# Performance work log

Hardware: AMD Instinct MI355X
Metric: run time of the kernel (lower is better)

The kernel has to match this reference:

```python
import jax, jax.numpy as jnp
import numpy as np

N_NODES = 512      # num_nodes (seq_len for LSTM, also output side length)
B = 64             # graph batch -> total nodes = B * N_NODES
T = B * N_NODES    # 32768 total nodes
E = 1048576        # edges before self-loops
D_IN = 128
H = 128
L = 2              # lstm layers


def setup_inputs() -> dict:
    key = jax.random.key(0)
    ks = jax.random.split(key, 12)
    x = jax.random.normal(ks[0], (T, D_IN), dtype=jnp.float32)
    edge_index = jax.random.randint(ks[1], (2, E), 0, T, dtype=jnp.int64)
    edge_weight = jax.random.uniform(ks[2], (E,), dtype=jnp.float32)
    batch = jax.random.randint(ks[3], (T,), 0, B, dtype=jnp.int64)
    s = 1.0 / np.sqrt(H)
    W_gcn = jax.random.normal(ks[4], (D_IN, H), dtype=jnp.float32) * s
    b_gcn = jnp.zeros((H,), dtype=jnp.float32)
    w_ih = jax.random.uniform(ks[5], (L, 4 * H, H), minval=-s, maxval=s, dtype=jnp.float32)
    w_hh = jax.random.uniform(ks[6], (L, 4 * H, H), minval=-s, maxval=s, dtype=jnp.float32)
    b_ih = jax.random.uniform(ks[7], (L, 4 * H), minval=-s, maxval=s, dtype=jnp.float32)
    b_hh = jax.random.uniform(ks[8], (L, 4 * H), minval=-s, maxval=s, dtype=jnp.float32)
    fc_w = jax.random.uniform(ks[9], (N_NODES * N_NODES, H), minval=-s, maxval=s, dtype=jnp.float32)
    fc_b = jax.random.uniform(ks[10], (N_NODES * N_NODES,), minval=-s, maxval=s, dtype=jnp.float32)
    return {"x": x, "edge_index": edge_index, "edge_weight": edge_weight, "batch": batch,
            "W_gcn": W_gcn, "b_gcn": b_gcn, "w_ih": w_ih, "w_hh": w_hh,
            "b_ih": b_ih, "b_hh": b_hh, "fc_w": fc_w, "fc_b": fc_b}


def _gcn_conv(x, edge_index, edge_weight, W, b):
    # PyG GCNConv with edge weights: add self-loops (w=1), symmetric norm, then aggregate.
    n = x.shape[0]
    loop = jnp.arange(n, dtype=edge_index.dtype)
    src = jnp.concatenate([edge_index[0], loop])
    dst = jnp.concatenate([edge_index[1], loop])
    w = jnp.concatenate([edge_weight, jnp.ones((n,), dtype=edge_weight.dtype)])
    deg = jax.ops.segment_sum(w, dst, num_segments=n)
    dinv = jnp.where(deg > 0, jax.lax.rsqrt(jnp.maximum(deg, 1e-30)), 0.0)
    norm = dinv[src] * w * dinv[dst]                  # [E+n]
    xw = x @ W                                        # [n, H]
    msg = norm[:, None] * xw[src]                     # gather + scale
    out = jax.ops.segment_sum(msg, dst, num_segments=n)  # scatter-add
    return out + b


def _lstm_layer(xs, wih, whh, bih, bhh):
    # xs: [S, B, H] time-major; torch gate order i,f,g,o.
    h0 = jnp.zeros((xs.shape[1], whh.shape[1]), dtype=xs.dtype)
    c0 = jnp.zeros_like(h0)
    def step(carry, xt):
        h, c = carry
        gates = xt @ wih.T + h @ whh.T + bih + bhh
        i, f, g, o = jnp.split(gates, 4, axis=-1)
        c = jax.nn.sigmoid(f) * c + jax.nn.sigmoid(i) * jnp.tanh(g)
        h = jax.nn.sigmoid(o) * jnp.tanh(c)
        return (h, c), h
    _, hs = jax.lax.scan(step, (h0, c0), xs)
    return hs


def reference(x, edge_index, edge_weight, batch, W_gcn, b_gcn, w_ih, w_hh, b_ih, b_hh, fc_w, fc_b):
    h = _gcn_conv(x, edge_index, edge_weight, W_gcn, b_gcn)   # [T, H]
    # split into chunks of num_nodes and stack -> [B, N_NODES, H]
    h = h.reshape(B, N_NODES, H)
    xs = jnp.transpose(h, (1, 0, 2))                           # [S, B, H]
    for l in range(L):
        xs = _lstm_layer(xs, w_ih[l], w_hh[l], b_ih[l], b_hh[l])
    last = xs[-1]                                              # [B, H]
    out = last @ fc_w.T + fc_b                                 # [B, N_NODES^2]
    return out.reshape(N_NODES, -1)
```

## Files before the change

### kernel.cpp

```cpp
#include <hip/hip_runtime.h>

#define TNODES 32768
#define NEDGE  1048576
#define HD     128
#define NG     512
#define NB     64
#define SEQ    512
#define FCN    262144

__global__ __launch_bounds__(256) void k_deg(const int* __restrict__ ei,
                                             const float* __restrict__ ew,
                                             float* __restrict__ deg,
                                             int* __restrict__ cnt) {
    int e = blockIdx.x * 256 + threadIdx.x;
    int d = ei[NEDGE + e];
    atomicAdd(&deg[d], ew[e]);
    atomicAdd(&cnt[d], 1);
}

__global__ __launch_bounds__(256) void k_dinv(float* __restrict__ deg) {
    int n = blockIdx.x * 256 + threadIdx.x;
    deg[n] = rsqrtf(deg[n] + 1.0f);
}

__global__ __launch_bounds__(1024) void k_scan(const int* __restrict__ cnt,
                                               int* __restrict__ offs) {
    __shared__ int sums[1024];
    int t = threadIdx.x;
    int base = t * 32;
    int local[32];
    int s = 0;
    #pragma unroll
    for (int j = 0; j < 32; ++j) { local[j] = s; s += cnt[base + j]; }
    sums[t] = s;
    __syncthreads();
    for (int off = 1; off < 1024; off <<= 1) {
        int v = sums[t];
        int u = (t >= off) ? sums[t - off] : 0;
        __syncthreads();
        sums[t] = v + u;
        __syncthreads();
    }
    int baseSum = (t == 0) ? 0 : sums[t - 1];
    #pragma unroll
    for (int j = 0; j < 32; ++j) offs[base + j] = baseSum + local[j];
    if (t == 1023) offs[TNODES] = sums[1023];
}

__global__ __launch_bounds__(256) void k_fill(const int* __restrict__ ei,
                                              const float* __restrict__ ew,
                                              const float* __restrict__ dinv,
                                              const int* __restrict__ offs,
                                              int* __restrict__ cursor,
                                              int* __restrict__ csrc,
                                              float* __restrict__ ca) {
    int e = blockIdx.x * 256 + threadIdx.x;
    int s = ei[e];
    int d = ei[NEDGE + e];
    int p = offs[d] + atomicAdd(&cursor[d], 1);
    csrc[p] = s;
    ca[p] = ew[e] * dinv[s];
}

__global__ __launch_bounds__(256) void k_transpose(const float* __restrict__ W,
                                                   float* __restrict__ Wt) {
    int t = blockIdx.x * 256 + threadIdx.x;
    int c = t >> 7, k = t & 127;
    Wt[t] = W[k * HD + c];
}

#define GS 140
__global__ __launch_bounds__(256) void k_gemm_bt(const float* __restrict__ A,
                                                 const float* __restrict__ Bt,
                                                 const float* __restrict__ b1,
                                                 const float* __restrict__ b2,
                                                 float* __restrict__ C, int G) {
    __shared__ __align__(16) float As[64 * GS];
    __shared__ __align__(16) float Bs[64 * GS];
    int r0 = blockIdx.x * 64;
    int g0 = blockIdx.y * 64;
    int tid = threadIdx.x;
    #pragma unroll
    for (int it = 0; it < 8; ++it) {
        int idx = tid + 256 * it;
        int r = idx >> 5, c4 = idx & 31;
        float4 va = ((const float4*)(A + (size_t)(r0 + r) * HD))[c4];
        *((float4*)&As[r * GS + c4 * 4]) = va;
        float4 vb = ((const float4*)(Bt + (size_t)(g0 + r) * HD))[c4];
        *((float4*)&Bs[r * GS + c4 * 4]) = vb;
    }
    __syncthreads();
    int i = tid >> 4;
    int j = tid & 15;
    float acc[4][4];
    #pragma unroll
    for (int a = 0; a < 4; ++a)
        #pragma unroll
        for (int b = 0; b < 4; ++b) acc[a][b] = 0.f;
    #pragma unroll 8
    for (int k4 = 0; k4 < 32; ++k4) {
        float4 av[4], bv[4];
        #pragma unroll
        for (int mi = 0; mi < 4; ++mi)
            av[mi] = *((const float4*)&As[(i + 16 * mi) * GS + k4 * 4]);
        #pragma unroll
        for (int ni = 0; ni < 4; ++ni)
            bv[ni] = *((const float4*)&Bs[(j + 16 * ni) * GS + k4 * 4]);
        #pragma unroll
        for (int mi = 0; mi < 4; ++mi)
            #pragma unroll
            for (int ni = 0; ni < 4; ++ni)
                acc[mi][ni] += (av[mi].x * bv[ni].x + av[mi].y * bv[ni].y) +
                               (av[mi].z * bv[ni].z + av[mi].w * bv[ni].w);
    }
    #pragma unroll
    for (int mi = 0; mi < 4; ++mi)
        #pragma unroll
        for (int ni = 0; ni < 4; ++ni) {
            int g = g0 + j + 16 * ni;
            float bias = (b1 ? b1[g] : 0.f) + (b2 ? b2[g] : 0.f);
            C[(size_t)(r0 + i + 16 * mi) * G + g] = acc[mi][ni] + bias;
        }
}

__global__ __launch_bounds__(128) void k_agg(const int* __restrict__ offs,
                                             const int* __restrict__ csrc,
                                             const float* __restrict__ ca,
                                             const float* __restrict__ xw,
                                             const float* __restrict__ dinv,
                                             const float* __restrict__ bg,
                                             float* __restrict__ hg) {
    int d = blockIdx.x;
    int t = threadIdx.x;
    int beg = offs[d], end = offs[d + 1];
    float acc = 0.f;
    int e = beg;
    for (; e + 3 < end; e += 4) {
        int s0 = csrc[e], s1 = csrc[e + 1], s2 = csrc[e + 2], s3 = csrc[e + 3];
        float a0 = ca[e], a1 = ca[e + 1], a2 = ca[e + 2], a3 = ca[e + 3];
        acc += a0 * xw[(size_t)s0 * HD + t];
        acc += a1 * xw[(size_t)s1 * HD + t];
        acc += a2 * xw[(size_t)s2 * HD + t];
        acc += a3 * xw[(size_t)s3 * HD + t];
    }
    for (; e < end; ++e) acc += ca[e] * xw[(size_t)csrc[e] * HD + t];
    float di = dinv[d];
    hg[(size_t)d * HD + t] = di * acc + di * di * xw[(size_t)d * HD + t] + bg[t];
}

__device__ __forceinline__ float sigm(float x) { return 1.f / (1.f + __expf(-x)); }
__device__ __forceinline__ float tanh_s(float x) {
    float e = __expf(-2.f * fabsf(x));
    float t = (1.f - e) / (1.f + e);
    return copysignf(t, x);
}

#define COMP(v, j) ((j) == 0 ? (v).x : ((j) == 1 ? (v).y : ((j) == 2 ? (v).z : (v).w)))

__global__ __launch_bounds__(512, 2) void k_lstm(const float* __restrict__ P,
                                                 const float* __restrict__ whh,
                                                 float* __restrict__ Hout,
                                                 float* __restrict__ lastOut) {
    __shared__ __align__(16) float lds[20608];
    float* h_sh = lds + 18432;
    int b = blockIdx.x, t = threadIdx.x;
    int c = t >> 7;
    int i = t & 127;

    float4 w[4][8];
    for (int cc = 0; cc < 4; ++cc) {
        const float4* src = (const float4*)(whh + (size_t)t * HD + 32 * cc);
        float4 tmp[8];
        #pragma unroll
        for (int q = 0; q < 8; ++q) tmp[q] = src[q];
        __syncthreads();
        #pragma unroll
        for (int q = 0; q < 8; ++q)
            *((float4*)(lds + t * 36 + 4 * q)) = tmp[q];
        __syncthreads();
        if (cc == c) {
            #pragma unroll
            for (int g = 0; g < 4; ++g)
                #pragma unroll
                for (int q = 0; q < 8; ++q)
                    w[g][q] = *((const float4*)(lds + (i + 128 * g) * 36 + 4 * q));
        }
    }
    __syncthreads();

    if (t < HD) h_sh[t] = 0.f;
    float cst = 0.f;
    const float* Pb = P + (size_t)b * SEQ * NG;
    float pi = 0.f, pf = 0.f, pg = 0.f, po = 0.f;
    if (t < HD) { pi = Pb[t]; pf = Pb[128 + t]; pg = Pb[256 + t]; po = Pb[384 + t]; }
    __syncthreads();

    for (int s = 0; s < SEQ; ++s) {
        float pi2 = 0.f, pf2 = 0.f, pg2 = 0.f, po2 = 0.f;
        if (t < HD && s + 1 < SEQ) {
            const float* Pn = Pb + (size_t)(s + 1) * NG;
            pi2 = Pn[t]; pf2 = Pn[128 + t]; pg2 = Pn[256 + t]; po2 = Pn[384 + t];
        }
        float hv = h_sh[32 * c + (t & 31)];
        float4 acc = {0.f, 0.f, 0.f, 0.f};
        #pragma unroll
        for (int k = 0; k < 32; ++k) {
            float h = __int_as_float(__builtin_amdgcn_readlane(__float_as_int(hv), k));
            acc.x = fmaf(COMP(w[0][k >> 2], k & 3), h, acc.x);
            acc.y = fmaf(COMP(w[1][k >> 2], k & 3), h, acc.y);
            acc.z = fmaf(COMP(w[2][k >> 2], k & 3), h, acc.z);
            acc.w = fmaf(COMP(w[3][k >> 2], k & 3), h, acc.w);
        }
        ((float4*)lds)[c * 128 + i] = acc;
        __syncthreads();

        if (t < HD) {
            float4 s0 = ((const float4*)lds)[t];
            float4 s1 = ((const float4*)lds)[128 + t];
            float4 s2 = ((const float4*)lds)[256 + t];
            float4 s3 = ((const float4*)lds)[384 + t];
            float gi = (s0.x + s1.x) + (s2.x + s3.x) + pi;
            float gf = (s0.y + s1.y) + (s2.y + s3.y) + pf;
            float gg = (s0.z + s1.z) + (s2.z + s3.z) + pg;
            float go = (s0.w + s1.w) + (s2.w + s3.w) + po;
            float i_ = sigm(gi), f_ = sigm(gf), g_ = tanh_s(gg), o_ = sigm(go);
            cst = fmaf(f_, cst, i_ * g_);
            float h = o_ * tanh_s(cst);
            h_sh[t] = h;
            if (Hout) Hout[((size_t)b * SEQ + s) * HD + t] = h;
            if (lastOut && s == SEQ - 1) lastOut[b * HD + t] = h;
        }
        pi = pi2; pf = pf2; pg = pg2; po = po2;
        __syncthreads();
    }
}

__global__ __launch_bounds__(256) void k_fc(const float* __restrict__ last,
                                            const float* __restrict__ fcw,
                                            const float* __restrict__ fcb,
                                            float* __restrict__ out) {
    __shared__ __align__(16) float l_sh[NB * HD];
    int tid = threadIdx.x;
    #pragma unroll
    for (int it = 0; it < 32; ++it) l_sh[tid + 256 * it] = last[tid + 256 * it];
    __syncthreads();
    int i = blockIdx.x * 256 + tid;
    const float4* wrow = (const float4*)(fcw + (size_t)i * HD);
    float acc[NB];
    #pragma unroll
    for (int b = 0; b < NB; ++b) acc[b] = 0.f;
    for (int k4 = 0; k4 < 32; ++k4) {
        float4 w4 = wrow[k4];
        #pragma unroll
        for (int b = 0; b < NB; ++b) {
            float4 l4 = ((const float4*)(l_sh + b * HD))[k4];
            acc[b] += (w4.x * l4.x + w4.y * l4.y) + (w4.z * l4.z + w4.w * l4.w);
        }
    }
    float bias = fcb[i];
    #pragma unroll
    for (int b = 0; b < NB; ++b) out[(size_t)b * FCN + i] = acc[b] + bias;
}

extern "C" void kernel_launch(void* const* d_in, const int* in_sizes, int n_in,
                              void* d_out, int out_size, void* d_ws, size_t ws_size,
                              hipStream_t stream) {
    const float* x   = (const float*)d_in[0];
    const int*   ei  = (const int*)d_in[1];
    const float* ew  = (const float*)d_in[2];
    const float* Wg  = (const float*)d_in[4];
    const float* bg  = (const float*)d_in[5];
    const float* wih = (const float*)d_in[6];
    const float* whh = (const float*)d_in[7];
    const float* bih = (const float*)d_in[8];
    const float* bhh = (const float*)d_in[9];
    const float* fcw = (const float*)d_in[10];
    const float* fcb = (const float*)d_in[11];
    float* out = (float*)d_out;

    float* ws = (float*)d_ws;
    float* deg    = ws;
    int*   cnt    = (int*)(ws + 32768);
    int*   cursor = (int*)(ws + 65536);
    int*   offs   = (int*)(ws + 98304);
    int*   csrc   = (int*)(ws + 131136);
    float* ca     = ws + 1179712;
    float* Wt     = ws + 2228288;
    float* xw     = ws + 2244672;
    float* hg     = ws + 6438976;
    float* H0     = ws + 10633280;
    float* lastb  = ws + 14827584;
    float* P      = ws + 14835776;

    hipMemsetAsync(d_ws, 0, 3 * 32768 * sizeof(float), stream);

    k_deg<<<NEDGE / 256, 256, 0, stream>>>(ei, ew, deg, cnt);
    k_dinv<<<TNODES / 256, 256, 0, stream>>>(deg);
    k_scan<<<1, 1024, 0, stream>>>(cnt, offs);
    k_fill<<<NEDGE / 256, 256, 0, stream>>>(ei, ew, deg, offs, cursor, csrc, ca);
    k_transpose<<<64, 256, 0, stream>>>(Wg, Wt);
    k_gemm_bt<<<dim3(TNODES / 64, HD / 64), 256, 0, stream>>>(x, Wt, nullptr, nullptr, xw, HD);
    k_agg<<<TNODES, 128, 0, stream>>>(offs, csrc, ca, xw, deg, bg, hg);

    k_gemm_bt<<<dim3(TNODES / 64, NG / 64), 256, 0, stream>>>(hg, wih, bih, bhh, P, NG);
    k_lstm<<<NB, 512, 0, stream>>>(P, whh, H0, nullptr);
    k_gemm_bt<<<dim3(TNODES / 64, NG / 64), 256, 0, stream>>>(H0, wih + 65536, bih + 512, bhh + 512, P, NG);
    k_lstm<<<NB, 512, 0, stream>>>(P, whh + 65536, nullptr, lastb);

    k_fc<<<FCN / 256, 256, 0, stream>>>(lastb, fcw, fcb, out);
}
```

Measured before the change: 1.651 ms.

## Split LSTM recurrent matvec across 1024 threads with 8-way K partition

The recurrent LSTM kernel goes from 512 to 1024 threads per block. The hidden dimension is now split into 8 chunks of 16 instead of 4 chunks of 32, so each thread keeps half as many W_hh registers and runs a 16-step readlane FMA loop instead of 32. This shortens the serial per-timestep critical path and eases register pressure. In exchange the gate reduction reads and sums 8 partials instead of 4, and each step synchronises twice as many waves.

```diff
diff --git a/kernel.cpp b/kernel.cpp
--- a/kernel.cpp
+++ b/kernel.cpp
@@ -157,33 +157,34 @@
 
 #define COMP(v, j) ((j) == 0 ? (v).x : ((j) == 1 ? (v).y : ((j) == 2 ? (v).z : (v).w)))
 
-__global__ __launch_bounds__(512, 2) void k_lstm(const float* __restrict__ P,
-                                                 const float* __restrict__ whh,
-                                                 float* __restrict__ Hout,
-                                                 float* __restrict__ lastOut) {
+__global__ __launch_bounds__(1024) void k_lstm(const float* __restrict__ P,
+                                               const float* __restrict__ whh,
+                                               float* __restrict__ Hout,
+                                               float* __restrict__ lastOut) {
     __shared__ __align__(16) float lds[20608];
-    float* h_sh = lds + 18432;
+    float* h_sh = lds + 4096;
     int b = blockIdx.x, t = threadIdx.x;
     int c = t >> 7;
     int i = t & 127;
 
-    float4 w[4][8];
-    for (int cc = 0; cc < 4; ++cc) {
-        const float4* src = (const float4*)(whh + (size_t)t * HD + 32 * cc);
-        float4 tmp[8];
-        #pragma unroll
-        for (int q = 0; q < 8; ++q) tmp[q] = src[q];
-        __syncthreads();
-        #pragma unroll
-        for (int q = 0; q < 8; ++q)
-            *((float4*)(lds + t * 36 + 4 * q)) = tmp[q];
-        __syncthreads();
-        if (cc == c) {
-            #pragma unroll
-            for (int g = 0; g < 4; ++g)
+    float4 w[4][4];
+    for (int p = 0; p < 8; ++p) {
+        for (int h2 = 0; h2 < 2; ++h2) {
+            int rl = t >> 2;
+            int q4 = (t & 3) * 4;
+            float4 v = *(const float4*)(whh + (size_t)(256 * h2 + rl) * HD + 16 * p + q4);
+            __syncthreads();
+            *(float4*)(lds + 4 * t) = v;
+            __syncthreads();
+            if (c == p) {
                 #pragma unroll
-                for (int q = 0; q < 8; ++q)
-                    w[g][q] = *((const float4*)(lds + (i + 128 * g) * 36 + 4 * q));
+                for (int gg = 0; gg < 2; ++gg) {
+                    int row = i + 128 * gg;
+                    #pragma unroll
+                    for (int q = 0; q < 4; ++q)
+                        w[2 * h2 + gg][q] = *(const float4*)(lds + row * 16 + 4 * q);
+                }
+            }
         }
     }
     __syncthreads();
@@ -201,10 +202,10 @@
             const float* Pn = Pb + (size_t)(s + 1) * NG;
             pi2 = Pn[t]; pf2 = Pn[128 + t]; pg2 = Pn[256 + t]; po2 = Pn[384 + t];
         }
-        float hv = h_sh[32 * c + (t & 31)];
+        float hv = h_sh[16 * c + (t & 15)];
         float4 acc = {0.f, 0.f, 0.f, 0.f};
         #pragma unroll
-        for (int k = 0; k < 32; ++k) {
+        for (int k = 0; k < 16; ++k) {
             float h = __int_as_float(__builtin_amdgcn_readlane(__float_as_int(hv), k));
             acc.x = fmaf(COMP(w[0][k >> 2], k & 3), h, acc.x);
             acc.y = fmaf(COMP(w[1][k >> 2], k & 3), h, acc.y);
@@ -219,10 +220,14 @@
             float4 s1 = ((const float4*)lds)[128 + t];
             float4 s2 = ((const float4*)lds)[256 + t];
             float4 s3 = ((const float4*)lds)[384 + t];
-            float gi = (s0.x + s1.x) + (s2.x + s3.x) + pi;
-            float gf = (s0.y + s1.y) + (s2.y + s3.y) + pf;
-            float gg = (s0.z + s1.z) + (s2.z + s3.z) + pg;
-            float go = (s0.w + s1.w) + (s2.w + s3.w) + po;
+            float4 s4 = ((const float4*)lds)[512 + t];
+            float4 s5 = ((const float4*)lds)[640 + t];
+            float4 s6 = ((const float4*)lds)[768 + t];
+            float4 s7 = ((const float4*)lds)[896 + t];
+            float gi = ((s0.x + s1.x) + (s2.x + s3.x)) + ((s4.x + s5.x) + (s6.x + s7.x)) + pi;
+            float gf = ((s0.y + s1.y) + (s2.y + s3.y)) + ((s4.y + s5.y) + (s6.y + s7.y)) + pf;
+            float gg = ((s0.z + s1.z) + (s2.z + s3.z)) + ((s4.z + s5.z) + (s6.z + s7.z)) + pg;
+            float go = ((s0.w + s1.w) + (s2.w + s3.w)) + ((s4.w + s5.w) + (s6.w + s7.w)) + po;
             float i_ = sigm(gi), f_ = sigm(gf), g_ = tanh_s(gg), o_ = sigm(go);
             cst = fmaf(f_, cst, i_ * g_);
             float h = o_ * tanh_s(cst);
@@ -303,9 +308,9 @@
     k_agg<<<TNODES, 128, 0, stream>>>(offs, csrc, ca, xw, deg, bg, hg);
 
     k_gemm_bt<<<dim3(TNODES / 64, NG / 64), 256, 0, stream>>>(hg, wih, bih, bhh, P, NG);
-    k_lstm<<<NB, 512, 0, stream>>>(P, whh, H0, nullptr);
+    k_lstm<<<NB, 1024, 0, stream>>>(P, whh, H0, nullptr);
     k_gemm_bt<<<dim3(TNODES / 64, NG / 64), 256, 0, stream>>>(H0, wih + 65536, bih + 512, bhh + 512, P, NG);
-    k_lstm<<<NB, 512, 0, stream>>>(P, whh + 65536, nullptr, lastb);
+    k_lstm<<<NB, 1024, 0, stream>>>(P, whh + 65536, nullptr, lastb);
 
     k_fc<<<FCN / 256, 256, 0, stream>>>(lastb, fcw, fcb, out);
 }
```

Result: slower. 1.696 ms (+2.7%).
